# Kernel optimization log

Hardware: AMD Instinct MI355X
Metric: run time of the kernel (lower is better)

The kernel has to match this reference:

```python
import jax, jax.numpy as jnp
import numpy as np
from itertools import combinations

N_KERNELS, KLEN = 84, 9
MAX_IN_LENGTH, IN_CHANNELS = 512, 3
HIDDEN_DIM, MAX_DIL_PER_KERNEL = 10000, 64
BATCH = 8


def _build_params():
    """Replicates Rocket.__init__: builds the dense 'massive' conv weight and bias."""
    hd = HIDDEN_DIM // IN_CHANNELS
    nfpk = hd // N_KERNELS                      # features per kernel
    tmax = min(nfpk, MAX_DIL_PER_KERNEL)
    mult = nfpk / tmax
    max_exp = np.log2((MAX_IN_LENGTH - 1) / (KLEN - 1))
    dilations, counts = np.unique(
        np.logspace(0, max_exp, tmax, base=2).astype(np.int32), return_counts=True)
    nfpd = (counts * mult).astype(np.int32)
    rem = nfpk - int(nfpd.sum())
    i = 0
    while rem > 0:
        nfpd[i] += 1
        rem -= 1
        i = (i + 1) % len(nfpd)
    # 84 base kernels: -1 everywhere, 2 at each 3-combination of 9 positions
    W84 = np.full((N_KERNELS, KLEN), -1.0, np.float32)
    beta = np.array(list(combinations(range(KLEN), 3)), np.int32)
    W84[np.arange(len(beta))[:, None], beta] = 2.0
    maxd = int(dilations.max())
    max_pad = 4 * maxd
    out_channels = N_KERNELS * int(nfpd.sum())
    K = KLEN * maxd
    big = np.zeros((out_channels, 1, K), np.float32)
    bias_blocks = []
    i = 0
    for d, n in zip(dilations.tolist(), nfpd.tolist()):
        excess = max_pad - 4 * d
        # bias set: (n, 84), each row a constant from linspace(-1, 1, n)
        bset = np.tile(np.linspace(-1, 1, n), N_KERNELS).reshape(N_KERNELS, n).T.astype(np.float32)
        for j in range(n):
            big[(i + j) * N_KERNELS:(i + j + 1) * N_KERNELS, 0,
                excess:excess + KLEN * d:d] = W84
        bias_blocks.append(bset)
        i += n
    bias = np.concatenate(bias_blocks, 0).reshape(-1)
    return jnp.asarray(big), jnp.asarray(bias)


def setup_inputs() -> dict:
    key = jax.random.key(0)
    X = jax.random.normal(key, (BATCH, IN_CHANNELS, MAX_IN_LENGTH), dtype=jnp.float32)
    W, b = _build_params()
    return {"X": X, "W": W, "b": b}


def reference(X, W, b):
    # X: (B, C, L); W: (O, 1, K) with K = 9*max_dilation; b: (O,)
    B, C, L = X.shape
    max_pad = (W.shape[-1] // KLEN) * 4  # 4 * max_dilation
    # each channel convolved independently with the same filter bank -> fold C into batch
    x = X.reshape(B * C, 1, L)
    out = jax.lax.conv_general_dilated(
        x, W, window_strides=(1,), padding=[(max_pad, max_pad)],
        dimension_numbers=("NCH", "OIH", "NCH"))
    out = out + b[None, :, None]
    # torch cats per-channel results along dim 1 -> (B, C*O, L_out)
    return out.reshape(B, C * W.shape[0], out.shape[-1])
```

## Files before the change

### kernel.cpp

```cpp
#include <hip/hip_runtime.h>

#define LN 512
#define NK 84
#define THREADS 256

__global__ void parse_groups(const float* __restrict__ W, int K, int maxd,
                             int n_groups, int* __restrict__ dil) {
    const int g = blockIdx.x;
    if (g >= n_groups) return;
    const int j = threadIdx.x;
    const float* row = W + (size_t)g * NK * K;
    float v = (j <= maxd && 4 * j < K) ? row[4 * j] : 0.0f;
    unsigned long long m = __ballot(v != 0.0f);
    int j0 = __ffsll((unsigned long long)m) - 1;
    if (j == 0) dil[g] = maxd - j0;
}

__global__ __launch_bounds__(THREADS) void rocket_main(
    const float* __restrict__ X, const float* __restrict__ bias,
    const int* __restrict__ dil, float* __restrict__ out,
    int O, int T, int max_pad, int n_groups) {
    extern __shared__ float xs[];

    const int g  = blockIdx.x % n_groups;
    const int bc = blockIdx.x / n_groups;

    for (int i = threadIdx.x; i < max_pad; i += THREADS) {
        xs[i] = 0.0f;
        xs[max_pad + LN + i] = 0.0f;
    }
    const float* xrow = X + (size_t)bc * LN;
    for (int i = threadIdx.x; i < LN; i += THREADS) {
        xs[max_pad + i] = xrow[i];
    }
    __syncthreads();

    const int   d  = dil[g];
    const float bv = bias[(size_t)g * NK];
    float* const outg = out + ((size_t)bc * O + (size_t)g * NK) * T;

    const int pairs = T >> 1;
    for (int p = threadIdx.x; p < pairs; p += THREADS) {
        const int t0   = 2 * p;
        const int base = max_pad + t0 - 4 * d;
        float tx[9], ty[9];
        float s9x = 0.0f, s9y = 0.0f;
#pragma unroll
        for (int j = 0; j < 9; ++j) {
            tx[j] = xs[base + j * d];
            ty[j] = xs[base + j * d + 1];
            s9x += tx[j];
            s9y += ty[j];
        }
        const float bx = bv - s9x;
        const float by = bv - s9y;

        float* op = outg + t0;
#pragma unroll
        for (int a = 0; a < 7; ++a) {
#pragma unroll
            for (int b2 = a + 1; b2 < 8; ++b2) {
                const float px = tx[a] + tx[b2];
                const float py = ty[a] + ty[b2];
#pragma unroll
                for (int c = b2 + 1; c < 9; ++c) {
                    const float ox = fmaf(3.0f, px + tx[c], bx);
                    const float oy = fmaf(3.0f, py + ty[c], by);
                    *(float2*)op = make_float2(ox, oy);
                    op += T;
                }
            }
        }
    }

    if ((T & 1) && threadIdx.x == 0) {
        const int t    = T - 1;
        const int base = max_pad + t - 4 * d;
        float tx[9]; float s9 = 0.0f;
#pragma unroll
        for (int j = 0; j < 9; ++j) { tx[j] = xs[base + j * d]; s9 += tx[j]; }
        const float bx = bv - s9;
        float* op = outg + t;
        for (int a = 0; a < 7; ++a)
            for (int b2 = a + 1; b2 < 8; ++b2)
                for (int c = b2 + 1; c < 9; ++c) {
                    *op = fmaf(3.0f, tx[a] + tx[b2] + tx[c], bx);
                    op += T;
                }
    }
}

extern "C" void kernel_launch(void* const* d_in, const int* in_sizes, int n_in,
                              void* d_out, int out_size, void* d_ws, size_t ws_size,
                              hipStream_t stream) {
    const float* X = (const float*)d_in[0];
    const float* W = (const float*)d_in[1];
    const float* b = (const float*)d_in[2];
    float* out = (float*)d_out;

    const int O        = in_sizes[2];
    const int K        = in_sizes[1] / O;
    const int maxd     = K / 9;
    const int max_pad  = 4 * maxd;
    const int BC       = in_sizes[0] / LN;
    const int T        = out_size / (BC * O);
    const int n_groups = O / NK;

    int* dil = (int*)d_ws;

    parse_groups<<<n_groups, 64, 0, stream>>>(W, K, maxd, n_groups, dil);

    const size_t smem = (size_t)(LN + 2 * max_pad + 4) * sizeof(float);
    rocket_main<<<BC * n_groups, THREADS, smem, stream>>>(
        X, b, dil, out, O, T, max_pad, n_groups);
}
```

Measured before the change: 151.3 us.

## Fuse dilation parsing into main kernel and use nontemporal stores

Drops the separate parse_groups launch: each block's first wavefront now reads the weight row itself and derives the dilation into shared memory. The inner loop precomputes 3*x+bias per tap, so each output takes one FMA instead of an add plus an FMA. Stores become nontemporal 64-bit writes with a byte-stride pointer, meant to keep the very large streaming output from polluting cache. The cost is redundant weight reads in every block, plus a dependency on the compiler honouring the nontemporal hint.

Result: slower. 164.8 us (+8.9%).

```diff
diff --git a/kernel.cpp b/kernel.cpp
--- a/kernel.cpp
+++ b/kernel.cpp
@@ -4,26 +4,23 @@
 #define NK 84
 #define THREADS 256
 
-__global__ void parse_groups(const float* __restrict__ W, int K, int maxd,
-                             int n_groups, int* __restrict__ dil) {
-    const int g = blockIdx.x;
-    if (g >= n_groups) return;
-    const int j = threadIdx.x;
-    const float* row = W + (size_t)g * NK * K;
-    float v = (j <= maxd && 4 * j < K) ? row[4 * j] : 0.0f;
-    unsigned long long m = __ballot(v != 0.0f);
-    int j0 = __ffsll((unsigned long long)m) - 1;
-    if (j == 0) dil[g] = maxd - j0;
-}
-
-__global__ __launch_bounds__(THREADS) void rocket_main(
-    const float* __restrict__ X, const float* __restrict__ bias,
-    const int* __restrict__ dil, float* __restrict__ out,
-    int O, int T, int max_pad, int n_groups) {
+__global__ __launch_bounds__(THREADS) void rocket_fused(
+    const float* __restrict__ X, const float* __restrict__ W,
+    const float* __restrict__ bias, float* __restrict__ out,
+    int O, int K, int T, int maxd, int max_pad, int n_groups) {
     extern __shared__ float xs[];
+    __shared__ int s_d;
 
     const int g  = blockIdx.x % n_groups;
     const int bc = blockIdx.x / n_groups;
+
+    if (threadIdx.x < 64) {
+        const int j = threadIdx.x;
+        const float* row = W + (size_t)g * NK * K;
+        float v = (j <= maxd && 4 * j < K) ? row[4 * j] : 0.0f;
+        unsigned long long m = __ballot(v != 0.0f);
+        if (j == 0) s_d = maxd - (__ffsll(m) - 1);
+    }
 
     for (int i = threadIdx.x; i < max_pad; i += THREADS) {
         xs[i] = 0.0f;
@@ -35,9 +32,10 @@
     }
     __syncthreads();
 
-    const int   d  = dil[g];
+    const int   d  = s_d;
     const float bv = bias[(size_t)g * NK];
     float* const outg = out + ((size_t)bc * O + (size_t)g * NK) * T;
+    const uint32_t stepb = (uint32_t)T * 4u;
 
     const int pairs = T >> 1;
     for (int p = threadIdx.x; p < pairs; p += THREADS) {
@@ -54,8 +52,14 @@
         }
         const float bx = bv - s9x;
         const float by = bv - s9y;
+        float qx[9], qy[9];
+#pragma unroll
+        for (int j = 0; j < 9; ++j) {
+            qx[j] = fmaf(3.0f, tx[j], bx);
+            qy[j] = fmaf(3.0f, ty[j], by);
+        }
 
-        float* op = outg + t0;
+        char* op = (char*)(outg + t0);
 #pragma unroll
         for (int a = 0; a < 7; ++a) {
 #pragma unroll
@@ -64,10 +68,11 @@
                 const float py = ty[a] + ty[b2];
 #pragma unroll
                 for (int c = b2 + 1; c < 9; ++c) {
-                    const float ox = fmaf(3.0f, px + tx[c], bx);
-                    const float oy = fmaf(3.0f, py + ty[c], by);
-                    *(float2*)op = make_float2(ox, oy);
-                    op += T;
+                    union { float2 f2; unsigned long long u; } u;
+                    u.f2 = make_float2(fmaf(3.0f, px, qx[c]),
+                                       fmaf(3.0f, py, qy[c]));
+                    __builtin_nontemporal_store(u.u, (unsigned long long*)op);
+                    op += stepb;
                 }
             }
         }
@@ -106,11 +111,7 @@
     const int T        = out_size / (BC * O);
     const int n_groups = O / NK;
 
-    int* dil = (int*)d_ws;
-
-    parse_groups<<<n_groups, 64, 0, stream>>>(W, K, maxd, n_groups, dil);
-
     const size_t smem = (size_t)(LN + 2 * max_pad + 4) * sizeof(float);
-    rocket_main<<<BC * n_groups, THREADS, smem, stream>>>(
-        X, b, dil, out, O, T, max_pad, n_groups);
+    rocket_fused<<<BC * n_groups, THREADS, smem, stream>>>(
+        X, W, b, out, O, K, T, maxd, max_pad, n_groups);
 }
```
